# Optimization experiments

Hardware: AMD Instinct MI355X
Metric: run time of the kernel (lower is better)

## Reference

```python
import jax, jax.numpy as jnp
import numpy as np

# Graph dimensions (homogeneous node ordering per hetero2homo: [function, input, output])
N_F, N_I, N_O = 2000, 500, 500
N = N_F + N_I + N_O
C = 8                 # hidden channels per function node
H = N_F * C           # total hidden width
B = 256
E_FF, E_IF, E_FO = 40000, 5000, 2000
E = E_FF + E_IF + E_FO
EPS = 1e-5


def _build_graph():
    rng = np.random.default_rng(0)
    src_ff = rng.integers(0, N_F, E_FF)
    dst_ff = rng.integers(0, N_F, E_FF)
    src_if = rng.integers(N_F, N_F + N_I, E_IF)          # input -> function
    dst_if = rng.integers(0, N_F, E_IF)
    src_fo = rng.integers(0, N_F, E_FO)                   # function -> output
    dst_fo = rng.integers(N_F + N_I, N, E_FO)
    src = np.concatenate([src_ff, src_if, src_fo])
    dst = np.concatenate([dst_ff, dst_if, dst_fo])
    edge_index = jnp.asarray(np.stack([src, dst]), dtype=jnp.int32)
    mask = np.zeros(N, dtype=bool)
    mask[N_F + N_I:] = True
    return edge_index, jnp.asarray(mask)


def setup_inputs() -> dict:
    key = jax.random.key(0)
    k_x, k_w1, k_b1, k_w2, k_b2 = jax.random.split(key, 5)
    edge_index, output_node_mask = _build_graph()
    scale = 0.1  # xavier-ish for small fan-in/out
    return {
        "x": jax.random.normal(k_x, (B, N), dtype=jnp.float32),
        "w1": jax.random.normal(k_w1, (E, C), dtype=jnp.float32) * scale,
        "b1": jax.random.normal(k_b1, (H,), dtype=jnp.float32) * 0.01,
        "gamma": jnp.ones((H,), dtype=jnp.float32),
        "beta": jnp.zeros((H,), dtype=jnp.float32),
        "w2": jax.random.normal(k_w2, (E, C), dtype=jnp.float32) * scale,
        "b2": jax.random.normal(k_b2, (E,), dtype=jnp.float32) * 0.01,
        "edge_index": edge_index,
        "output_node_mask": output_node_mask,
        "layers": 10,
    }


def reference(x, w1, b1, gamma, beta, w2, b2, edge_index, output_node_mask, layers):
    src, dst = edge_index[0], edge_index[1]
    # W_in structure: hidden channel k of function node n receives edge e iff dst[e]==n.
    # Edges whose dst is not a function node are structurally absent -> route to dummy segment N_F.
    dst_seg = jnp.where(dst < N_F, dst, N_F)
    # W_out structure: edge e receives hidden channels of function node src[e]; zero otherwise.
    src_is_func = src < N_F
    src_clip = jnp.where(src_is_func, src, 0)

    xe = x[:, src]  # node2edge: (B, E)
    for _ in range(layers):
        # lin_in: sparse (E x H) matmul == per-edge outer product scatter-added onto dst node channels
        contrib = xe.T[:, :, None] * w1[:, None, :]                       # (E, B, C)
        hid = jax.ops.segment_sum(contrib, dst_seg, num_segments=N_F + 1)[:N_F]  # (N_F, B, C)
        h = hid.transpose(1, 0, 2).reshape(B, H) + b1                      # (B, H)
        # layer norm then nonlin (norm_first=True)
        mu = h.mean(-1, keepdims=True)
        var = h.var(-1, keepdims=True)
        h = (h - mu) * jax.lax.rsqrt(var + EPS) * gamma + beta
        h = jax.nn.elu(h)
        # lin_out: sparse (H x E) matmul == gather src-node channels, dot with per-edge weights
        hn = h.reshape(B, N_F, C)
        out_e = jnp.einsum('bec,ec->be', hn[:, src_clip, :], w2)
        out_e = jnp.where(src_is_func[None, :], out_e, 0.0) + b2[None, :]
        xe = xe + out_e                                                    # residual
    xe = xe / layers
    # edge2node: scatter-add edge features onto output nodes only
    xm = jnp.where(output_node_mask[dst][None, :], xe, 0.0)
    out = jax.ops.segment_sum(xm.T, dst, num_segments=output_node_mask.shape[0]).T  # (B, N)
    return out
```

## Files before the change

### kernel.cpp

```cpp
#include <hip/hip_runtime.h>
#include <cmath>

#define N_F    2000
#define N_ALL  3000
#define N_SRC  2500
#define OUT0   2500
#define C      8
#define H      16000
#define B      256
#define E      47000
#define LAYERS 10
#define EPSF   1e-5f
#define CHK    64
#define SB     250
#define SR     64


__global__ void k_zero(int* cnt_dst, int* cnt_src) {
    int tid = threadIdx.x;
    for (int i = tid; i < N_ALL; i += 1024) { cnt_dst[i] = 0; cnt_src[i] = 0; }
}

__global__ void k_count(const int* __restrict__ src, const int* __restrict__ dst,
                        int* cnt_dst, int* cnt_src) {
    int e = blockIdx.x * 256 + threadIdx.x;
    if (e < E) {
        atomicAdd(&cnt_dst[dst[e]], 1);
        atomicAdd(&cnt_src[src[e]], 1);
    }
}

__global__ void k_scan(const int* cnt_dst, const int* cnt_src,
                       int* rs_dst, int* rs_src, int* cur_dst, int* cur_src) {
    const int* cnt = (blockIdx.x == 0) ? cnt_dst : cnt_src;
    int* rs  = (blockIdx.x == 0) ? rs_dst : rs_src;
    int* cur = (blockIdx.x == 0) ? cur_dst : cur_src;
    __shared__ int buf[1024];
    __shared__ int carry;
    int tid = threadIdx.x;
    if (tid == 0) carry = 0;
    __syncthreads();
    for (int base = 0; base < N_ALL; base += 1024) {
        int i = base + tid;
        int v = (i < N_ALL) ? cnt[i] : 0;
        buf[tid] = v;
        __syncthreads();
        for (int off = 1; off < 1024; off <<= 1) {
            int t = (tid >= off) ? buf[tid - off] : 0;
            __syncthreads();
            buf[tid] += t;
            __syncthreads();
        }
        int excl = carry + buf[tid] - v;
        if (i < N_ALL) { rs[i] = excl; cur[i] = excl; }
        int tot = buf[1023];
        __syncthreads();
        if (tid == 0) carry += tot;
        __syncthreads();
    }
    if (tid == 0) rs[N_ALL] = carry;
}

__global__ void k_fill(const int* __restrict__ src, const int* __restrict__ dst,
                       int* cur_dst, int* cur_src, int* csr_dst, int* csr_src) {
    int e = blockIdx.x * 256 + threadIdx.x;
    if (e < E) {
        int p = atomicAdd(&cur_dst[dst[e]], 1); csr_dst[p] = e;
        int q = atomicAdd(&cur_src[src[e]], 1); csr_src[q] = e;
    }
}


__global__ void k_xT(const float* __restrict__ x, float* __restrict__ xT) {
    __shared__ float t[32][33];
    int tx = threadIdx.x, ty = threadIdx.y;
    int n = blockIdx.x * 32 + tx, b = blockIdx.y * 32 + ty;
    if (n < N_ALL) t[ty][tx] = x[b * N_ALL + n];
    __syncthreads();
    int n2 = blockIdx.x * 32 + ty, b2 = blockIdx.y * 32 + tx;
    if (n2 < N_ALL) xT[n2 * B + b2] = t[tx][ty];
}

__global__ void k_init(const int* __restrict__ src, const float* __restrict__ xT,
                       float* __restrict__ xe) {
    int tid = threadIdx.x;
    int e0 = blockIdx.x * 16;
    for (int k = 0; k < 16; ++k) {
        int e = e0 + k;
        if (e < E) {
            int s = src[e];
            xe[e * B + tid] = xT[s * B + tid];
        }
    }
}


__global__ void k_hid(const float* __restrict__ xe, const float* __restrict__ w1,
                      const int* __restrict__ rs_dst, const int* __restrict__ csr_dst,
                      float* __restrict__ h) {
    int n = blockIdx.x, tid = threadIdx.x;
    int beg = rs_dst[n], end = rs_dst[n + 1];
    float acc[C] = {0.f, 0.f, 0.f, 0.f, 0.f, 0.f, 0.f, 0.f};
    __shared__ int   eid[CHK];
    __shared__ float w1s[CHK][C];
    for (int cb = beg; cb < end; cb += CHK) {
        int m = min(CHK, end - cb);
        if (tid < m) eid[tid] = csr_dst[cb + tid];
        __syncthreads();
        for (int idx = tid; idx < m * C; idx += B) {
            int j = idx >> 3, c = idx & 7;
            w1s[j][c] = w1[eid[j] * C + c];
        }
        __syncthreads();
        for (int j = 0; j < m; ++j) {
            float xv = xe[eid[j] * B + tid];
            #pragma unroll
            for (int c = 0; c < C; ++c) acc[c] += xv * w1s[j][c];
        }
        __syncthreads();
    }
    #pragma unroll
    for (int c = 0; c < C; ++c) h[(n * C + c) * B + tid] = acc[c];
}

__global__ void k_stats(const float* __restrict__ h, const float* __restrict__ b1,
                        float* __restrict__ part) {
    int tid = threadIdx.x;
    int b = tid & 255, rg = tid >> 8;
    int r0 = blockIdx.x * SR;
    float s1 = 0.f, s2 = 0.f;
    for (int r = rg; r < SR; r += 4) {
        int i = r0 + r;
        float v = h[i * B + b] + b1[i];
        s1 += v; s2 += v * v;
    }
    __shared__ float l1[4][B], l2[4][B];
    l1[rg][b] = s1; l2[rg][b] = s2;
    __syncthreads();
    if (rg == 0) {
        float a = l1[0][b] + l1[1][b] + l1[2][b] + l1[3][b];
        float q = l2[0][b] + l2[1][b] + l2[2][b] + l2[3][b];
        part[blockIdx.x * (2 * B) + b]     = a;
        part[blockIdx.x * (2 * B) + B + b] = q;
    }
}

__global__ void k_norm(float* __restrict__ h, const float* __restrict__ part,
                       const float* __restrict__ b1, const float* __restrict__ gamma,
                       const float* __restrict__ beta) {
    int tid = threadIdx.x;
    int b = tid & 255, rg = tid >> 8;
    float s1 = 0.f, s2 = 0.f;
    for (int k = rg; k < SB; k += 4) {
        s1 += part[k * (2 * B) + b];
        s2 += part[k * (2 * B) + B + b];
    }
    __shared__ float l1[4][B], l2[4][B], mu_s[B], rs_s[B];
    l1[rg][b] = s1; l2[rg][b] = s2;
    __syncthreads();
    if (rg == 0) {
        float S1 = l1[0][b] + l1[1][b] + l1[2][b] + l1[3][b];
        float S2 = l2[0][b] + l2[1][b] + l2[2][b] + l2[3][b];
        float mu = S1 * (1.0f / H);
        float var = S2 * (1.0f / H) - mu * mu;
        mu_s[b] = mu;
        rs_s[b] = rsqrtf(var + EPSF);
    }
    __syncthreads();
    float mu = mu_s[b], rs = rs_s[b];
    int r0 = blockIdx.x * SR;
    for (int r = rg; r < SR; r += 4) {
        int i = r0 + r;
        float v = h[i * B + b] + b1[i];
        v = (v - mu) * rs * gamma[i] + beta[i];
        h[i * B + b] = (v > 0.f) ? v : expm1f(v);
    }
}

__global__ void k_edge(const float* __restrict__ h, const float* __restrict__ w2,
                       const float* __restrict__ b2, const int* __restrict__ rs_src,
                       const int* __restrict__ csr_src, float* __restrict__ xe) {
    int s = blockIdx.x, tid = threadIdx.x;
    int beg = rs_src[s], end = rs_src[s + 1];
    if (beg >= end) return;
    if (s < N_F) {
        float hv[C];
        #pragma unroll
        for (int c = 0; c < C; ++c) hv[c] = h[(s * C + c) * B + tid];
        __shared__ int   eid[CHK];
        __shared__ float w2s[CHK][C];
        __shared__ float b2s[CHK];
        for (int cb = beg; cb < end; cb += CHK) {
            int m = min(CHK, end - cb);
            if (tid < m) eid[tid] = csr_src[cb + tid];
            __syncthreads();
            for (int idx = tid; idx < m * C; idx += B) {
                int j = idx >> 3, c = idx & 7;
                w2s[j][c] = w2[eid[j] * C + c];
            }
            if (tid < m) b2s[tid] = b2[eid[tid]];
            __syncthreads();
            for (int j = 0; j < m; ++j) {
                float d = b2s[j];
                #pragma unroll
                for (int c = 0; c < C; ++c) d += hv[c] * w2s[j][c];
                xe[eid[j] * B + tid] += d;
            }
            __syncthreads();
        }
    } else {
        for (int j = beg; j < end; ++j) {
            int e = csr_src[j];
            xe[e * B + tid] += b2[e];
        }
    }
}

__global__ void k_out(const float* __restrict__ xe, const int* __restrict__ rs_dst,
                      const int* __restrict__ csr_dst, float* __restrict__ out) {
    int n = blockIdx.x, b = threadIdx.x;
    float v = 0.f;
    if (n >= OUT0) {
        int beg = rs_dst[n], end = rs_dst[n + 1];
        for (int j = beg; j < end; ++j) v += xe[csr_dst[j] * B + b];
    }
    out[b * N_ALL + n] = v * (1.0f / LAYERS);
}


extern "C" void kernel_launch(void* const* d_in, const int* in_sizes, int n_in,
                              void* d_out, int out_size, void* d_ws, size_t ws_size,
                              hipStream_t stream) {
    const float* x     = (const float*)d_in[0];
    const float* w1    = (const float*)d_in[1];
    const float* b1    = (const float*)d_in[2];
    const float* gamma = (const float*)d_in[3];
    const float* beta  = (const float*)d_in[4];
    const float* w2    = (const float*)d_in[5];
    const float* b2    = (const float*)d_in[6];
    const int*   ei    = (const int*)d_in[7];
    const int* src = ei;
    const int* dst = ei + E;
    float* out = (float*)d_out;

    char* p = (char*)d_ws;
    float* xe = (float*)p; p += (size_t)E * B * sizeof(float);
    float* xT = (float*)p; p += (size_t)N_ALL * B * sizeof(float);
    float* h  = (float*)p; p += (size_t)H * B * sizeof(float);
    float* part = (float*)p; p += (size_t)SB * 2 * B * sizeof(float);
    int* cnt_dst = (int*)p; p += N_ALL * sizeof(int);
    int* cnt_src = (int*)p; p += N_ALL * sizeof(int);
    int* rs_dst  = (int*)p; p += (N_ALL + 1) * sizeof(int);
    int* rs_src  = (int*)p; p += (N_ALL + 1) * sizeof(int);
    int* cur_dst = (int*)p; p += N_ALL * sizeof(int);
    int* cur_src = (int*)p; p += N_ALL * sizeof(int);
    int* csr_dst = (int*)p; p += E * sizeof(int);
    int* csr_src = (int*)p; p += E * sizeof(int);

    hipLaunchKernelGGL(k_zero,  dim3(1), dim3(1024), 0, stream, cnt_dst, cnt_src);
    hipLaunchKernelGGL(k_count, dim3((E + 255) / 256), dim3(256), 0, stream, src, dst, cnt_dst, cnt_src);
    hipLaunchKernelGGL(k_scan,  dim3(2), dim3(1024), 0, stream, cnt_dst, cnt_src, rs_dst, rs_src, cur_dst, cur_src);
    hipLaunchKernelGGL(k_fill,  dim3((E + 255) / 256), dim3(256), 0, stream, src, dst, cur_dst, cur_src, csr_dst, csr_src);
    hipLaunchKernelGGL(k_xT,    dim3((N_ALL + 31) / 32, B / 32), dim3(32, 32), 0, stream, x, xT);
    hipLaunchKernelGGL(k_init,  dim3((E + 15) / 16), dim3(256), 0, stream, src, xT, xe);

    for (int t = 0; t < LAYERS; ++t) {
        hipLaunchKernelGGL(k_hid,   dim3(N_F), dim3(256), 0, stream, xe, w1, rs_dst, csr_dst, h);
        hipLaunchKernelGGL(k_stats, dim3(SB), dim3(1024), 0, stream, h, b1, part);
        hipLaunchKernelGGL(k_norm,  dim3(SB), dim3(1024), 0, stream, h, part, b1, gamma, beta);
        hipLaunchKernelGGL(k_edge,  dim3(N_SRC), dim3(256), 0, stream, h, w2, b2, rs_src, csr_src, xe);
    }

    hipLaunchKernelGGL(k_out, dim3(N_ALL), dim3(256), 0, stream, xe, rs_dst, csr_dst, out);
}
```

Before: 779.7 us.

## Reformulate layer recurrence algebraically and fuse all layers into one cooperative kernel

The per-edge state xe (E×B) is replaced by an algebraic decomposition. A constant base term from the input edges and b2 is precomputed once. Each layer then only handles function-to-function edge contributions q = w2·S, where S is the running sum of ELU outputs. All layers run in a single cooperative kernel with grid syncs, which removes most per-layer launches and xe traffic. Edge lists are split by edge type and sorted so accumulation order is deterministic, and a multi-kernel fallback is used when cooperative residency is not possible. The risks are grid.sync overhead, and low parallelism from 500 blocks each handling 4 nodes serially.

```diff
diff --git a/kernel.cpp b/kernel.cpp
--- a/kernel.cpp
+++ b/kernel.cpp
@@ -1,48 +1,59 @@
 #include <hip/hip_runtime.h>
+#include <hip/hip_cooperative_groups.h>
 #include <cmath>
+#include <cstdint>
+
+namespace cg = cooperative_groups;
 
 #define N_F    2000
+#define N_I    500
+#define N_O    500
 #define N_ALL  3000
-#define N_SRC  2500
-#define OUT0   2500
 #define C      8
 #define H      16000
 #define B      256
-#define E      47000
+#define E_FF   40000
+#define E_IF   5000
+#define E_FO   2000
+#define E_ALL  47000
 #define LAYERS 10
 #define EPSF   1e-5f
-#define CHK    64
-#define SB     250
-#define SR     64
-
-
-__global__ void k_zero(int* cnt_dst, int* cnt_src) {
+#define NBLK   500
+#define NPB    4
+
+
+__global__ void k_zero_cnt(int* cntA, int* cntB, int* cntC, int* cntD) {
     int tid = threadIdx.x;
-    for (int i = tid; i < N_ALL; i += 1024) { cnt_dst[i] = 0; cnt_src[i] = 0; }
+    for (int i = tid; i < N_F; i += 1024) { cntA[i] = 0; cntB[i] = 0; cntC[i] = 0; }
+    for (int i = tid; i < N_O; i += 1024) cntD[i] = 0;
 }
 
 __global__ void k_count(const int* __restrict__ src, const int* __restrict__ dst,
-                        int* cnt_dst, int* cnt_src) {
+                        int* cntA, int* cntB, int* cntC, int* cntD) {
     int e = blockIdx.x * 256 + threadIdx.x;
-    if (e < E) {
-        atomicAdd(&cnt_dst[dst[e]], 1);
-        atomicAdd(&cnt_src[src[e]], 1);
-    }
-}
-
-__global__ void k_scan(const int* cnt_dst, const int* cnt_src,
-                       int* rs_dst, int* rs_src, int* cur_dst, int* cur_src) {
-    const int* cnt = (blockIdx.x == 0) ? cnt_dst : cnt_src;
-    int* rs  = (blockIdx.x == 0) ? rs_dst : rs_src;
-    int* cur = (blockIdx.x == 0) ? cur_dst : cur_src;
+    if (e >= E_ALL) return;
+    int s = src[e], d = dst[e];
+    if (e < E_FF)             { atomicAdd(&cntA[d], 1); atomicAdd(&cntB[d], 1); atomicAdd(&cntC[s], 1); }
+    else if (e < E_FF + E_IF) { atomicAdd(&cntA[d], 1); }
+    else                      { atomicAdd(&cntD[d - (N_F + N_I)], 1); }
+}
+
+__global__ void k_scan(const int* cntA, const int* cntB, const int* cntC, const int* cntD,
+                       int* rsA, int* rsB, int* rsC, int* rsD,
+                       int* curA, int* curB, int* curC, int* curD) {
+    const int* cnt; int* rs; int* cur; int len;
+    if      (blockIdx.x == 0) { cnt = cntA; rs = rsA; cur = curA; len = N_F; }
+    else if (blockIdx.x == 1) { cnt = cntB; rs = rsB; cur = curB; len = N_F; }
+    else if (blockIdx.x == 2) { cnt = cntC; rs = rsC; cur = curC; len = N_F; }
+    else                      { cnt = cntD; rs = rsD; cur = curD; len = N_O; }
     __shared__ int buf[1024];
     __shared__ int carry;
     int tid = threadIdx.x;
     if (tid == 0) carry = 0;
     __syncthreads();
-    for (int base = 0; base < N_ALL; base += 1024) {
-        int i = base + tid;
-        int v = (i < N_ALL) ? cnt[i] : 0;
+    for (int base0 = 0; base0 < len; base0 += 1024) {
+        int i = base0 + tid;
+        int v = (i < len) ? cnt[i] : 0;
         buf[tid] = v;
         __syncthreads();
         for (int off = 1; off < 1024; off <<= 1) {
@@ -52,21 +63,47 @@
             __syncthreads();
         }
         int excl = carry + buf[tid] - v;
-        if (i < N_ALL) { rs[i] = excl; cur[i] = excl; }
+        if (i < len) { rs[i] = excl; cur[i] = excl; }
         int tot = buf[1023];
         __syncthreads();
         if (tid == 0) carry += tot;
         __syncthreads();
     }
-    if (tid == 0) rs[N_ALL] = carry;
+    if (tid == 0) rs[len] = carry;
 }
 
 __global__ void k_fill(const int* __restrict__ src, const int* __restrict__ dst,
-                       int* cur_dst, int* cur_src, int* csr_dst, int* csr_src) {
+                       int* curA, int* curB, int* curC, int* curD,
+                       int* eidA, int* eidB, int* eidC, int* eidD) {
     int e = blockIdx.x * 256 + threadIdx.x;
-    if (e < E) {
-        int p = atomicAdd(&cur_dst[dst[e]], 1); csr_dst[p] = e;
-        int q = atomicAdd(&cur_src[src[e]], 1); csr_src[q] = e;
+    if (e >= E_ALL) return;
+    int s = src[e], d = dst[e];
+    if (e < E_FF) {
+        int a = atomicAdd(&curA[d], 1); eidA[a] = e;
+        int j = atomicAdd(&curB[d], 1); eidB[j] = e;
+        int p = atomicAdd(&curC[s], 1); eidC[p] = e;
+    } else if (e < E_FF + E_IF) {
+        int a = atomicAdd(&curA[d], 1); eidA[a] = e;
+    } else {
+        int k = atomicAdd(&curD[d - (N_F + N_I)], 1); eidD[k] = e;
+    }
+}
+
+__global__ void k_sort(const int* rsA, int* eidA, const int* rsB, int* eidB,
+                       const int* rsC, int* eidC, const int* rsD, int* eidD) {
+    int t = blockIdx.x * 256 + threadIdx.x;
+    const int* rs; int* eid; int n;
+    if      (t < 2000) { rs = rsA; eid = eidA; n = t; }
+    else if (t < 4000) { rs = rsB; eid = eidB; n = t - 2000; }
+    else if (t < 6000) { rs = rsC; eid = eidC; n = t - 4000; }
+    else if (t < 6500) { rs = rsD; eid = eidD; n = t - 6000; }
+    else return;
+    int beg = rs[n], end = rs[n + 1];
+    for (int i = beg + 1; i < end; ++i) {
+        int key = eid[i];
+        int j = i - 1;
+        while (j >= beg && eid[j] > key) { eid[j + 1] = eid[j]; --j; }
+        eid[j + 1] = key;
     }
 }
 
@@ -81,152 +118,260 @@
     if (n2 < N_ALL) xT[n2 * B + b2] = t[tx][ty];
 }
 
-__global__ void k_init(const int* __restrict__ src, const float* __restrict__ xT,
-                       float* __restrict__ xe) {
-    int tid = threadIdx.x;
-    int e0 = blockIdx.x * 16;
-    for (int k = 0; k < 16; ++k) {
-        int e = e0 + k;
-        if (e < E) {
-            int s = src[e];
-            xe[e * B + tid] = xT[s * B + tid];
-        }
-    }
-}
-
-
-__global__ void k_hid(const float* __restrict__ xe, const float* __restrict__ w1,
-                      const int* __restrict__ rs_dst, const int* __restrict__ csr_dst,
-                      float* __restrict__ h) {
+__global__ void k_base(const float* __restrict__ xT, const float* __restrict__ w1,
+                       const float* __restrict__ b1, const float* __restrict__ b2,
+                       const int* __restrict__ rsA, const int* __restrict__ eidA,
+                       const int* __restrict__ srcv,
+                       float* __restrict__ baseG, float* __restrict__ bbG) {
     int n = blockIdx.x, tid = threadIdx.x;
-    int beg = rs_dst[n], end = rs_dst[n + 1];
-    float acc[C] = {0.f, 0.f, 0.f, 0.f, 0.f, 0.f, 0.f, 0.f};
-    __shared__ int   eid[CHK];
-    __shared__ float w1s[CHK][C];
-    for (int cb = beg; cb < end; cb += CHK) {
-        int m = min(CHK, end - cb);
-        if (tid < m) eid[tid] = csr_dst[cb + tid];
-        __syncthreads();
-        for (int idx = tid; idx < m * C; idx += B) {
-            int j = idx >> 3, c = idx & 7;
-            w1s[j][c] = w1[eid[j] * C + c];
-        }
-        __syncthreads();
-        for (int j = 0; j < m; ++j) {
-            float xv = xe[eid[j] * B + tid];
+    int beg = rsA[n], end = rsA[n + 1];
+    float acc[C] = {0.f,0.f,0.f,0.f,0.f,0.f,0.f,0.f};
+    float bba[C] = {0.f,0.f,0.f,0.f,0.f,0.f,0.f,0.f};
+    const float4* w14 = (const float4*)w1;
+    for (int a = beg; a < end; ++a) {
+        int e = eidA[a];
+        float xv = xT[srcv[e] * B + tid];
+        float bv = b2[e];
+        float4 u0 = w14[e * 2], u1 = w14[e * 2 + 1];
+        acc[0] += u0.x * xv; acc[1] += u0.y * xv; acc[2] += u0.z * xv; acc[3] += u0.w * xv;
+        acc[4] += u1.x * xv; acc[5] += u1.y * xv; acc[6] += u1.z * xv; acc[7] += u1.w * xv;
+        bba[0] += u0.x * bv; bba[1] += u0.y * bv; bba[2] += u0.z * bv; bba[3] += u0.w * bv;
+        bba[4] += u1.x * bv; bba[5] += u1.y * bv; bba[6] += u1.z * bv; bba[7] += u1.w * bv;
+    }
+    #pragma unroll
+    for (int c = 0; c < C; ++c) baseG[(n * C + c) * B + tid] = acc[c] + b1[n * C + c];
+    if (tid == 0) {
+        #pragma unroll
+        for (int c = 0; c < C; ++c) bbG[n * C + c] = bba[c];
+    }
+}
+
+
+__global__ __launch_bounds__(256, 2) void k_coop(
+    const float* __restrict__ xT, const float* __restrict__ w1,
+    const float* __restrict__ gamma, const float* __restrict__ beta,
+    const float* __restrict__ w2, const float* __restrict__ b2,
+    const int* __restrict__ srcv,
+    const int* __restrict__ rsB, const int* __restrict__ eidB,
+    const int* __restrict__ rsC, const int* __restrict__ eidC,
+    const int* __restrict__ rsD, const int* __restrict__ eidD,
+    const float* __restrict__ baseG, const float* __restrict__ bbG,
+    float* __restrict__ q, float* __restrict__ bp, float* __restrict__ p2,
+    float* __restrict__ Sg, float* __restrict__ out)
+{
+    cg::grid_group grid = cg::this_grid();
+    const int blk = blockIdx.x, tid = threadIdx.x;
+    const float4* w14 = (const float4*)w1;
+    const float4* w24 = (const float4*)w2;
+
+    #pragma unroll
+    for (int k2 = 0; k2 < 6; ++k2) out[blk * 1536 + k2 * 256 + tid] = 0.f;
+
+    float Sreg[NPB][C], hidR[NPB][C];
+
+    for (int t = 0; t < LAYERS; ++t) {
+        float tf = (float)t;
+        float s1 = 0.f, s2 = 0.f;
+        for (int u = 0; u < NPB; ++u) {
+            int n = blk * NPB + u;
             #pragma unroll
-            for (int c = 0; c < C; ++c) acc[c] += xv * w1s[j][c];
-        }
-        __syncthreads();
-    }
+            for (int c = 0; c < C; ++c)
+                hidR[u][c] = baseG[(n * C + c) * B + tid] + tf * bbG[n * C + c];
+            if (t > 0) {
+                int beg = rsB[n], end = rsB[n + 1];
+                for (int j = beg; j < end; ++j) {
+                    int e = eidB[j];
+                    float qv = q[e * B + tid];
+                    float4 u0 = w14[e * 2], u1 = w14[e * 2 + 1];
+                    hidR[u][0] += u0.x * qv; hidR[u][1] += u0.y * qv;
+                    hidR[u][2] += u0.z * qv; hidR[u][3] += u0.w * qv;
+                    hidR[u][4] += u1.x * qv; hidR[u][5] += u1.y * qv;
+                    hidR[u][6] += u1.z * qv; hidR[u][7] += u1.w * qv;
+                }
+            }
+            #pragma unroll
+            for (int c = 0; c < C; ++c) { s1 += hidR[u][c]; s2 += hidR[u][c] * hidR[u][c]; }
+        }
+        bp[(blk * 2 + 0) * B + tid] = s1;
+        bp[(blk * 2 + 1) * B + tid] = s2;
+        grid.sync();
+
+        if (blk < 8) {
+            float a1 = 0.f, a2 = 0.f;
+            for (int i = blk; i < NBLK; i += 8) {
+                a1 += bp[(i * 2 + 0) * B + tid];
+                a2 += bp[(i * 2 + 1) * B + tid];
+            }
+            p2[(blk * 2 + 0) * B + tid] = a1;
+            p2[(blk * 2 + 1) * B + tid] = a2;
+        }
+        grid.sync();
+
+        float S1 = 0.f, S2 = 0.f;
+        #pragma unroll
+        for (int k = 0; k < 8; ++k) {
+            S1 += p2[(k * 2 + 0) * B + tid];
+            S2 += p2[(k * 2 + 1) * B + tid];
+        }
+        float mu  = S1 * (1.0f / H);
+        float var = S2 * (1.0f / H) - mu * mu;
+        float rsq = rsqrtf(var + EPSF);
+        for (int u = 0; u < NPB; ++u) {
+            int n = blk * NPB + u;
+            #pragma unroll
+            for (int c = 0; c < C; ++c) {
+                float v = (hidR[u][c] - mu) * rsq * gamma[n * C + c] + beta[n * C + c];
+                v = (v > 0.f) ? v : expm1f(v);
+                Sreg[u][c] = (t == 0) ? v : (Sreg[u][c] + v);
+            }
+            if (t < LAYERS - 1) {
+                int beg = rsC[n], end = rsC[n + 1];
+                for (int p = beg; p < end; ++p) {
+                    int e = eidC[p];
+                    float4 u0 = w24[e * 2], u1 = w24[e * 2 + 1];
+                    float qv = u0.x * Sreg[u][0] + u0.y * Sreg[u][1] + u0.z * Sreg[u][2] + u0.w * Sreg[u][3]
+                             + u1.x * Sreg[u][4] + u1.y * Sreg[u][5] + u1.z * Sreg[u][6] + u1.w * Sreg[u][7];
+                    q[e * B + tid] = qv;
+                }
+            } else {
+                #pragma unroll
+                for (int c = 0; c < C; ++c) Sg[(n * C + c) * B + tid] = Sreg[u][c];
+            }
+        }
+        grid.sync();
+    }
+
+    {
+        int o = blk;
+        float acc = 0.f;
+        int beg = rsD[o], end = rsD[o + 1];
+        for (int k = beg; k < end; ++k) {
+            int e = eidD[k];
+            int s = srcv[e];
+            float4 u0 = w24[e * 2], u1 = w24[e * 2 + 1];
+            float dot = u0.x * Sg[(s * C + 0) * B + tid] + u0.y * Sg[(s * C + 1) * B + tid]
+                      + u0.z * Sg[(s * C + 2) * B + tid] + u0.w * Sg[(s * C + 3) * B + tid]
+                      + u1.x * Sg[(s * C + 4) * B + tid] + u1.y * Sg[(s * C + 5) * B + tid]
+                      + u1.z * Sg[(s * C + 6) * B + tid] + u1.w * Sg[(s * C + 7) * B + tid];
+            acc += xT[s * B + tid] + dot + (float)LAYERS * b2[e];
+        }
+        out[tid * N_ALL + (N_F + N_I + o)] = acc * (1.0f / LAYERS);
+    }
+}
+
+
+__global__ void f_hidstat(const float* __restrict__ baseG, const float* __restrict__ bbG,
+                          const float* __restrict__ w1, const float* __restrict__ q,
+                          const int* __restrict__ rsB, const int* __restrict__ eidB,
+                          float* __restrict__ hidG, float* __restrict__ bp, int t) {
+    int blk = blockIdx.x, tid = threadIdx.x;
+    const float4* w14 = (const float4*)w1;
+    float tf = (float)t;
+    float s1 = 0.f, s2 = 0.f;
+    for (int u = 0; u < NPB; ++u) {
+        int n = blk * NPB + u;
+        float hid[C];
+        #pragma unroll
+        for (int c = 0; c < C; ++c) hid[c] = baseG[(n * C + c) * B + tid] + tf * bbG[n * C + c];
+        if (t > 0) {
+            int beg = rsB[n], end = rsB[n + 1];
+            for (int j = beg; j < end; ++j) {
+                int e = eidB[j];
+                float qv = q[e * B + tid];
+                float4 u0 = w14[e * 2], u1 = w14[e * 2 + 1];
+                hid[0] += u0.x * qv; hid[1] += u0.y * qv; hid[2] += u0.z * qv; hid[3] += u0.w * qv;
+                hid[4] += u1.x * qv; hid[5] += u1.y * qv; hid[6] += u1.z * qv; hid[7] += u1.w * qv;
+            }
+        }
+        #pragma unroll
+        for (int c = 0; c < C; ++c) {
+            hidG[(n * C + c) * B + tid] = hid[c];
+            s1 += hid[c]; s2 += hid[c] * hid[c];
+        }
+    }
+    bp[(blk * 2 + 0) * B + tid] = s1;
+    bp[(blk * 2 + 1) * B + tid] = s2;
+}
+
+__global__ void f_red(const float* __restrict__ bp, float* __restrict__ p2) {
+    int blk = blockIdx.x, tid = threadIdx.x;
+    float a1 = 0.f, a2 = 0.f;
+    for (int i = blk; i < NBLK; i += 8) {
+        a1 += bp[(i * 2 + 0) * B + tid];
+        a2 += bp[(i * 2 + 1) * B + tid];
+    }
+    p2[(blk * 2 + 0) * B + tid] = a1;
+    p2[(blk * 2 + 1) * B + tid] = a2;
+}
+
+__global__ void f_upd(const float* __restrict__ hidG, const float* __restrict__ p2,
+                      const float* __restrict__ gamma, const float* __restrict__ beta,
+                      const float* __restrict__ w2, const int* __restrict__ rsC,
+                      const int* __restrict__ eidC,
+                      float* __restrict__ Sg, float* __restrict__ q, int t) {
+    int blk = blockIdx.x, tid = threadIdx.x;
+    const float4* w24 = (const float4*)w2;
+    float S1 = 0.f, S2 = 0.f;
     #pragma unroll
-    for (int c = 0; c < C; ++c) h[(n * C + c) * B + tid] = acc[c];
-}
-
-__global__ void k_stats(const float* __restrict__ h, const float* __restrict__ b1,
-                        float* __restrict__ part) {
-    int tid = threadIdx.x;
-    int b = tid & 255, rg = tid >> 8;
-    int r0 = blockIdx.x * SR;
-    float s1 = 0.f, s2 = 0.f;
-    for (int r = rg; r < SR; r += 4) {
-        int i = r0 + r;
-        float v = h[i * B + b] + b1[i];
-        s1 += v; s2 += v * v;
-    }
-    __shared__ float l1[4][B], l2[4][B];
-    l1[rg][b] = s1; l2[rg][b] = s2;
-    __syncthreads();
-    if (rg == 0) {
-        float a = l1[0][b] + l1[1][b] + l1[2][b] + l1[3][b];
-        float q = l2[0][b] + l2[1][b] + l2[2][b] + l2[3][b];
-        part[blockIdx.x * (2 * B) + b]     = a;
-        part[blockIdx.x * (2 * B) + B + b] = q;
-    }
-}
-
-__global__ void k_norm(float* __restrict__ h, const float* __restrict__ part,
-                       const float* __restrict__ b1, const float* __restrict__ gamma,
-                       const float* __restrict__ beta) {
-    int tid = threadIdx.x;
-    int b = tid & 255, rg = tid >> 8;
-    float s1 = 0.f, s2 = 0.f;
-    for (int k = rg; k < SB; k += 4) {
-        s1 += part[k * (2 * B) + b];
-        s2 += part[k * (2 * B) + B + b];
-    }
-    __shared__ float l1[4][B], l2[4][B], mu_s[B], rs_s[B];
-    l1[rg][b] = s1; l2[rg][b] = s2;
-    __syncthreads();
-    if (rg == 0) {
-        float S1 = l1[0][b] + l1[1][b] + l1[2][b] + l1[3][b];
-        float S2 = l2[0][b] + l2[1][b] + l2[2][b] + l2[3][b];
-        float mu = S1 * (1.0f / H);
-        float var = S2 * (1.0f / H) - mu * mu;
-        mu_s[b] = mu;
-        rs_s[b] = rsqrtf(var + EPSF);
-    }
-    __syncthreads();
-    float mu = mu_s[b], rs = rs_s[b];
-    int r0 = blockIdx.x * SR;
-    for (int r = rg; r < SR; r += 4) {
-        int i = r0 + r;
-        float v = h[i * B + b] + b1[i];
-        v = (v - mu) * rs * gamma[i] + beta[i];
-        h[i * B + b] = (v > 0.f) ? v : expm1f(v);
-    }
-}
-
-__global__ void k_edge(const float* __restrict__ h, const float* __restrict__ w2,
-                       const float* __restrict__ b2, const int* __restrict__ rs_src,
-                       const int* __restrict__ csr_src, float* __restrict__ xe) {
-    int s = blockIdx.x, tid = threadIdx.x;
-    int beg = rs_src[s], end = rs_src[s + 1];
-    if (beg >= end) return;
-    if (s < N_F) {
-        float hv[C];
-        #pragma unroll
-        for (int c = 0; c < C; ++c) hv[c] = h[(s * C + c) * B + tid];
-        __shared__ int   eid[CHK];
-        __shared__ float w2s[CHK][C];
-        __shared__ float b2s[CHK];
-        for (int cb = beg; cb < end; cb += CHK) {
-            int m = min(CHK, end - cb);
-            if (tid < m) eid[tid] = csr_src[cb + tid];
-            __syncthreads();
-            for (int idx = tid; idx < m * C; idx += B) {
-                int j = idx >> 3, c = idx & 7;
-                w2s[j][c] = w2[eid[j] * C + c];
-            }
-            if (tid < m) b2s[tid] = b2[eid[tid]];
-            __syncthreads();
-            for (int j = 0; j < m; ++j) {
-                float d = b2s[j];
-                #pragma unroll
-                for (int c = 0; c < C; ++c) d += hv[c] * w2s[j][c];
-                xe[eid[j] * B + tid] += d;
-            }
-            __syncthreads();
-        }
-    } else {
-        for (int j = beg; j < end; ++j) {
-            int e = csr_src[j];
-            xe[e * B + tid] += b2[e];
-        }
-    }
-}
-
-__global__ void k_out(const float* __restrict__ xe, const int* __restrict__ rs_dst,
-                      const int* __restrict__ csr_dst, float* __restrict__ out) {
-    int n = blockIdx.x, b = threadIdx.x;
-    float v = 0.f;
-    if (n >= OUT0) {
-        int beg = rs_dst[n], end = rs_dst[n + 1];
-        for (int j = beg; j < end; ++j) v += xe[csr_dst[j] * B + b];
-    }
-    out[b * N_ALL + n] = v * (1.0f / LAYERS);
-}
-
+    for (int k = 0; k < 8; ++k) {
+        S1 += p2[(k * 2 + 0) * B + tid];
+        S2 += p2[(k * 2 + 1) * B + tid];
+    }
+    float mu  = S1 * (1.0f / H);
+    float var = S2 * (1.0f / H) - mu * mu;
+    float rsq = rsqrtf(var + EPSF);
+    for (int u = 0; u < NPB; ++u) {
+        int n = blk * NPB + u;
+        float Sn[C];
+        #pragma unroll
+        for (int c = 0; c < C; ++c) {
+            float v = (hidG[(n * C + c) * B + tid] - mu) * rsq * gamma[n * C + c] + beta[n * C + c];
+            v = (v > 0.f) ? v : expm1f(v);
+            Sn[c] = (t == 0) ? v : (Sg[(n * C + c) * B + tid] + v);
+        }
+        #pragma unroll
+        for (int c = 0; c < C; ++c) Sg[(n * C + c) * B + tid] = Sn[c];
+        if (t < LAYERS - 1) {
+            int beg = rsC[n], end = rsC[n + 1];
+            for (int p = beg; p < end; ++p) {
+                int e = eidC[p];
+                float4 u0 = w24[e * 2], u1 = w24[e * 2 + 1];
+                float qv = u0.x * Sn[0] + u0.y * Sn[1] + u0.z * Sn[2] + u0.w * Sn[3]
+                         + u1.x * Sn[4] + u1.y * Sn[5] + u1.z * Sn[6] + u1.w * Sn[7];
+                q[e * B + tid] = qv;
+            }
+        }
+    }
+}
+
+__global__ void f_zero_out(float* __restrict__ out) {
+    int i = blockIdx.x * 256 + threadIdx.x;
+    ((float4*)out)[i] = make_float4(0.f, 0.f, 0.f, 0.f);
+}
+
+__global__ void f_out(const float* __restrict__ xT, const float* __restrict__ Sg,
+                      const int* __restrict__ rsD, const int* __restrict__ eidD,
+                      const int* __restrict__ srcv, const float* __restrict__ w2,
+                      const float* __restrict__ b2, float* __restrict__ out) {
+    int o = blockIdx.x, tid = threadIdx.x;
+    const float4* w24 = (const float4*)w2;
+    float acc = 0.f;
+    int beg = rsD[o], end = rsD[o + 1];
+    for (int k = beg; k < end; ++k) {
+        int e = eidD[k];
+        int s = srcv[e];
+        float4 u0 = w24[e * 2], u1 = w24[e * 2 + 1];
+        float dot = u0.x * Sg[(s * C + 0) * B + tid] + u0.y * Sg[(s * C + 1) * B + tid]
+                  + u0.z * Sg[(s * C + 2) * B + tid] + u0.w * Sg[(s * C + 3) * B + tid]
+                  + u1.x * Sg[(s * C + 4) * B + tid] + u1.y * Sg[(s * C + 5) * B + tid]
+                  + u1.z * Sg[(s * C + 6) * B + tid] + u1.w * Sg[(s * C + 7) * B + tid];
+        acc += xT[s * B + tid] + dot + (float)LAYERS * b2[e];
+    }
+    out[tid * N_ALL + (N_F + N_I + o)] = acc * (1.0f / LAYERS);
+}
+
+
+static inline char* alignup(char* p) { return (char*)(((uintptr_t)p + 255) & ~(uintptr_t)255); }
 
 extern "C" void kernel_launch(void* const* d_in, const int* in_sizes, int n_in,
                               void* d_out, int out_size, void* d_ws, size_t ws_size,
@@ -239,37 +384,76 @@
     const float* w2    = (const float*)d_in[5];
     const float* b2    = (const float*)d_in[6];
     const int*   ei    = (const int*)d_in[7];
-    const int* src = ei;
-    const int* dst = ei + E;
+    const int* srcv = ei;
+    const int* dstv = ei + E_ALL;
     float* out = (float*)d_out;
 
     char* p = (char*)d_ws;
-    float* xe = (float*)p; p += (size_t)E * B * sizeof(float);
-    float* xT = (float*)p; p += (size_t)N_ALL * B * sizeof(float);
-    float* h  = (float*)p; p += (size_t)H * B * sizeof(float);
-    float* part = (float*)p; p += (size_t)SB * 2 * B * sizeof(float);
-    int* cnt_dst = (int*)p; p += N_ALL * sizeof(int);
-    int* cnt_src = (int*)p; p += N_ALL * sizeof(int);
-    int* rs_dst  = (int*)p; p += (N_ALL + 1) * sizeof(int);
-    int* rs_src  = (int*)p; p += (N_ALL + 1) * sizeof(int);
-    int* cur_dst = (int*)p; p += N_ALL * sizeof(int);
-    int* cur_src = (int*)p; p += N_ALL * sizeof(int);
-    int* csr_dst = (int*)p; p += E * sizeof(int);
-    int* csr_src = (int*)p; p += E * sizeof(int);
-
-    hipLaunchKernelGGL(k_zero,  dim3(1), dim3(1024), 0, stream, cnt_dst, cnt_src);
-    hipLaunchKernelGGL(k_count, dim3((E + 255) / 256), dim3(256), 0, stream, src, dst, cnt_dst, cnt_src);
-    hipLaunchKernelGGL(k_scan,  dim3(2), dim3(1024), 0, stream, cnt_dst, cnt_src, rs_dst, rs_src, cur_dst, cur_src);
-    hipLaunchKernelGGL(k_fill,  dim3((E + 255) / 256), dim3(256), 0, stream, src, dst, cur_dst, cur_src, csr_dst, csr_src);
-    hipLaunchKernelGGL(k_xT,    dim3((N_ALL + 31) / 32, B / 32), dim3(32, 32), 0, stream, x, xT);
-    hipLaunchKernelGGL(k_init,  dim3((E + 15) / 16), dim3(256), 0, stream, src, xT, xe);
-
-    for (int t = 0; t < LAYERS; ++t) {
-        hipLaunchKernelGGL(k_hid,   dim3(N_F), dim3(256), 0, stream, xe, w1, rs_dst, csr_dst, h);
-        hipLaunchKernelGGL(k_stats, dim3(SB), dim3(1024), 0, stream, h, b1, part);
-        hipLaunchKernelGGL(k_norm,  dim3(SB), dim3(1024), 0, stream, h, part, b1, gamma, beta);
-        hipLaunchKernelGGL(k_edge,  dim3(N_SRC), dim3(256), 0, stream, h, w2, b2, rs_src, csr_src, xe);
-    }
-
-    hipLaunchKernelGGL(k_out, dim3(N_ALL), dim3(256), 0, stream, xe, rs_dst, csr_dst, out);
-}
+    float* q     = (float*)p; p += (size_t)E_FF * B * 4;    p = alignup(p);
+    float* Sg    = (float*)p; p += (size_t)H * B * 4;       p = alignup(p);
+    float* baseG = (float*)p; p += (size_t)H * B * 4;       p = alignup(p);
+    float* hidG  = (float*)p; p += (size_t)H * B * 4;       p = alignup(p);
+    float* xT    = (float*)p; p += (size_t)N_ALL * B * 4;   p = alignup(p);
+    float* bp    = (float*)p; p += (size_t)NBLK * 2 * B * 4; p = alignup(p);
+    float* p2    = (float*)p; p += 8 * 2 * B * 4;           p = alignup(p);
+    float* bbG   = (float*)p; p += (size_t)N_F * C * 4;     p = alignup(p);
+    int* cntA = (int*)p; p += N_F * 4;        p = alignup(p);
+    int* cntB = (int*)p; p += N_F * 4;        p = alignup(p);
+    int* cntC = (int*)p; p += N_F * 4;        p = alignup(p);
+    int* cntD = (int*)p; p += N_O * 4;        p = alignup(p);
+    int* curA = (int*)p; p += N_F * 4;        p = alignup(p);
+    int* curB = (int*)p; p += N_F * 4;        p = alignup(p);
+    int* curC = (int*)p; p += N_F * 4;        p = alignup(p);
+    int* curD = (int*)p; p += N_O * 4;        p = alignup(p);
+    int* rsA  = (int*)p; p += (N_F + 1) * 4;  p = alignup(p);
+    int* rsB  = (int*)p; p += (N_F + 1) * 4;  p = alignup(p);
+    int* rsC  = (int*)p; p += (N_F + 1) * 4;  p = alignup(p);
+    int* rsD  = (int*)p; p += (N_O + 1) * 4;  p = alignup(p);
+    int* eidA = (int*)p; p += (size_t)(E_FF + E_IF) * 4; p = alignup(p);
+    int* eidB = (int*)p; p += (size_t)E_FF * 4; p = alignup(p);
+    int* eidC = (int*)p; p += (size_t)E_FF * 4; p = alignup(p);
+    int* eidD = (int*)p; p += (size_t)E_FO * 4; p = alignup(p);
+
+    hipLaunchKernelGGL(k_zero_cnt, dim3(1), dim3(1024), 0, stream, cntA, cntB, cntC, cntD);
+    hipLaunchKernelGGL(k_count, dim3((E_ALL + 255) / 256), dim3(256), 0, stream,
+                       srcv, dstv, cntA, cntB, cntC, cntD);
+    hipLaunchKernelGGL(k_scan, dim3(4), dim3(1024), 0, stream,
+                       cntA, cntB, cntC, cntD, rsA, rsB, rsC, rsD, curA, curB, curC, curD);
+    hipLaunchKernelGGL(k_fill, dim3((E_ALL + 255) / 256), dim3(256), 0, stream,
+                       srcv, dstv, curA, curB, curC, curD, eidA, eidB, eidC, eidD);
+    hipLaunchKernelGGL(k_sort, dim3(26), dim3(256), 0, stream,
+                       rsA, eidA, rsB, eidB, rsC, eidC, rsD, eidD);
+    hipLaunchKernelGGL(k_xT, dim3((N_ALL + 31) / 32, B / 32), dim3(32, 32), 0, stream, x, xT);
+    hipLaunchKernelGGL(k_base, dim3(N_F), dim3(256), 0, stream,
+                       xT, w1, b1, b2, rsA, eidA, srcv, baseG, bbG);
+
+    int dev = 0;
+    (void)hipGetDevice(&dev);
+    int numCU = 0;
+    (void)hipDeviceGetAttribute(&numCU, hipDeviceAttributeMultiprocessorCount, dev);
+    int maxPerCU = 0;
+    (void)hipOccupancyMaxActiveBlocksPerMultiprocessor(&maxPerCU, (const void*)k_coop, 256, 0);
+    bool coop_ok = (maxPerCU > 0) && ((long)maxPerCU * (long)numCU >= NBLK);
+
+    if (coop_ok) {
+        void* args[] = {
+            (void*)&xT, (void*)&w1, (void*)&gamma, (void*)&beta,
+            (void*)&w2, (void*)&b2, (void*)&srcv,
+            (void*)&rsB, (void*)&eidB, (void*)&rsC, (void*)&eidC,
+            (void*)&rsD, (void*)&eidD, (void*)&baseG, (void*)&bbG,
+            (void*)&q, (void*)&bp, (void*)&p2, (void*)&Sg, (void*)&out
+        };
+        hipLaunchCooperativeKernel((void*)k_coop, dim3(NBLK), dim3(256), args, 0, stream);
+    } else {
+        hipLaunchKernelGGL(f_zero_out, dim3(750), dim3(256), 0, stream, out);
+        for (int t = 0; t < LAYERS; ++t) {
+            hipLaunchKernelGGL(f_hidstat, dim3(NBLK), dim3(256), 0, stream,
+                               baseG, bbG, w1, q, rsB, eidB, hidG, bp, t);
+            hipLaunchKernelGGL(f_red, dim3(8), dim3(256), 0, stream, bp, p2);
+            hipLaunchKernelGGL(f_upd, dim3(NBLK), dim3(256), 0, stream,
+                               hidG, p2, gamma, beta, w2, rsC, eidC, Sg, q, t);
+        }
+        hipLaunchKernelGGL(f_out, dim3(N_O), dim3(256), 0, stream,
+                           xT, Sg, rsD, eidD, srcv, w2, b2, out);
+    }
+}
```

Result: slower. 1.202 ms (+54.2%).
